# Performance work log

Hardware: AMD Instinct MI355X
Metric: run time of the kernel (lower is better)

The kernel has to match this reference:

```python
import jax, jax.numpy as jnp
import numpy as np

LEN = 8388608  # 2**23, must be a power of 2


def setup_inputs() -> dict:
    key = jax.random.key(0)
    k1, k2 = jax.random.split(key)
    inp = jax.random.normal(k1, (LEN,), dtype=jnp.float32)
    weight = jax.random.uniform(k2, (LEN // 2, 2), dtype=jnp.float32)  # learned twiddle factors
    return {"input": inp, "weight": weight}


def _complex_mul(a, w):
    # a: [d, cols, 2] complex pairs; w: [cols, 2] broadcast over leading dim
    ar, ai = a[:, :, 0], a[:, :, 1]
    wr, wi = w[:, 0], w[:, 1]
    return jnp.stack([ar * wr - ai * wi, ar * wi + ai * wr], axis=-1)


def reference(input, weight):
    n = input.shape[0]
    # real signal -> complex pairs, shape [n, 1, 2]
    x = jnp.stack([input, jnp.zeros_like(input)], axis=-1)[:, None, :]
    d = n // 2
    while d != 0:  # log2(n) static stages
        w = weight[0::d]          # [cols, 2] where cols == x.shape[1]
        top = x[:d]               # [d, cols, 2]
        bot = x[d:]               # [d, cols, 2]
        p = _complex_mul(bot, w)  # butterfly twiddle multiply
        x = jnp.concatenate([top + p, top - p], axis=1)  # [d, 2*cols, 2]
        d //= 2
    return x  # [1, n, 2]
```

## Files before the change

### kernel.cpp

```cpp
#include <hip/hip_runtime.h>
#include <hip/hip_fp16.h>

__device__ __forceinline__ float2 cadd(float2 a, float2 b) { return make_float2(a.x + b.x, a.y + b.y); }
__device__ __forceinline__ float2 csub(float2 a, float2 b) { return make_float2(a.x - b.x, a.y - b.y); }
__device__ __forceinline__ float2 cmul(float2 w, float2 z) {
    return make_float2(w.x * z.x - w.y * z.y, w.x * z.y + w.y * z.x);
}
__device__ __forceinline__ unsigned pk(float2 z) {
    __half2 h = __floats2half2_rn(z.x, z.y);
    return *reinterpret_cast<unsigned*>(&h);
}
__device__ __forceinline__ float2 upk(unsigned u) {
    __half2 h = *reinterpret_cast<__half2*>(&u);
    return __half22float2(h);
}


__global__ __launch_bounds__(256) void fft_pass_a(const float* __restrict__ in,
                                                  const float2* __restrict__ wt,
                                                  uint4* __restrict__ outp)
{
    __shared__ float2 L[4096];
    const int tid = threadIdx.x;
    const int l0  = blockIdx.x << 4;
    const int c   = tid & 15;
    const int qb  = tid >> 4;

    float2 pw1[4], pw2a[4], pw2b[4];
#pragma unroll
    for (int k = 0; k < 4; ++k) { pw1[k] = wt[0]; pw2a[k] = wt[0]; pw2b[k] = wt[1 << 21]; }

    {
        const int c4 = tid & 3, gg = tid >> 2;
#pragma unroll
        for (int k = 0; k < 4; ++k) {
            const int g = gg + (k << 6);
            const float4 v = *reinterpret_cast<const float4*>(in + ((size_t)g << 15) + l0 + (c4 << 2));
            const int base = (g << 4) + (c4 << 2);
            L[base + 0] = make_float2(v.x, 0.f);
            L[base + 1] = make_float2(v.y, 0.f);
            L[base + 2] = make_float2(v.z, 0.f);
            L[base + 3] = make_float2(v.w, 0.f);
        }
    }
    __syncthreads();

#pragma unroll
    for (int rho = 0; rho < 4; ++rho) {
        const int s = rho << 1, H = 128 >> s, Q = H >> 1, lo = 6 - s;
        float2 nw1[4], nw2a[4], nw2b[4];
        if (rho < 3) {
            const int s2 = s + 2, lo2 = 6 - s2;
#pragma unroll
            for (int k = 0; k < 4; ++k) {
                const int qi = (qb << 2) + k;
                const int b  = ((qi >> lo2) << (lo2 + 2)) | (qi & ((1 << lo2) - 1));
                const int jl = (int)(__brev((unsigned)(b >> (8 - s2))) >> (32 - s2));
                const int e  = jl << (21 - s2);
                nw1[k] = wt[e << 1]; nw2a[k] = wt[e]; nw2b[k] = wt[e + (1 << 21)];
            }
        }
#pragma unroll
        for (int k = 0; k < 4; ++k) {
            const int qi = (qb << 2) + k;
            const int b  = ((qi >> lo) << (lo + 2)) | (qi & ((1 << lo) - 1));
            const int iA = (b << 4) + c;
            const float2 A  = L[iA];
            const float2 Bv = L[iA + (Q << 4)];
            const float2 Cv = L[iA + (H << 4)];
            const float2 Dv = L[iA + ((H + Q) << 4)];
            const float2 pC = cmul(pw1[k], Cv), pD = cmul(pw1[k], Dv);
            const float2 tA = cadd(A, pC),  tC = csub(A, pC);
            const float2 tB = cadd(Bv, pD), tD = csub(Bv, pD);
            const float2 p2 = cmul(pw2a[k], tB);
            const float2 p3 = cmul(pw2b[k], tD);
            L[iA]                  = cadd(tA, p2);
            L[iA + (Q << 4)]       = csub(tA, p2);
            L[iA + (H << 4)]       = cadd(tC, p3);
            L[iA + ((H + Q) << 4)] = csub(tC, p3);
        }
        __syncthreads();
        if (rho < 3) {
#pragma unroll
            for (int k = 0; k < 4; ++k) { pw1[k] = nw1[k]; pw2a[k] = nw2a[k]; pw2b[k] = nw2b[k]; }
        }
    }

    {
        const int c4 = tid & 3, gg = tid >> 2;
#pragma unroll
        for (int k = 0; k < 4; ++k) {
            const int g  = gg + (k << 6);
            const int li = (g << 4) + (c4 << 2);
            uint4 v;
            v.x = pk(L[li]); v.y = pk(L[li + 1]); v.z = pk(L[li + 2]); v.w = pk(L[li + 3]);
            outp[((size_t)g << 13) + (l0 >> 2) + c4] = v;
        }
    }
}

__global__ __launch_bounds__(256) void fft_pass_b(const uint4* __restrict__ inp,
                                                  const float2* __restrict__ wt,
                                                  uint4* __restrict__ outp)
{
    __shared__ float2 L[4096];
    const int tid  = threadIdx.x;
    const int h    = blockIdx.x >> 3;
    const int l0   = (blockIdx.x & 7) << 4;
    const int hrev = (int)(__brev((unsigned)h) >> 24);
    const int c  = tid & 15;
    const int qb = tid >> 4;
    const size_t pbase = ((size_t)h << 13) + (l0 >> 2);

    float2 pw1[4], pw2a[4], pw2b[4];
    {
        const int e0 = hrev << 13;
#pragma unroll
        for (int k = 0; k < 4; ++k) { pw1[k] = wt[e0 << 1]; pw2a[k] = wt[e0]; pw2b[k] = wt[e0 + (1 << 21)]; }
    }

    {
        const int c4 = tid & 3, gg = tid >> 2;
#pragma unroll
        for (int k = 0; k < 4; ++k) {
            const int g = gg + (k << 6);
            const uint4 v = inp[pbase + (g << 5) + c4];
            const int li = (g << 4) + (c4 << 2);
            L[li]     = upk(v.x);
            L[li + 1] = upk(v.y);
            L[li + 2] = upk(v.z);
            L[li + 3] = upk(v.w);
        }
    }
    __syncthreads();

#pragma unroll
    for (int rho = 0; rho < 4; ++rho) {
        const int s = rho << 1, H = 128 >> s, Q = H >> 1, lo = 6 - s;
        float2 nw1[4], nw2a[4], nw2b[4];
        if (rho < 3) {
            const int s2 = s + 2, lo2 = 6 - s2;
#pragma unroll
            for (int k = 0; k < 4; ++k) {
                const int qi = (qb << 2) + k;
                const int b  = ((qi >> lo2) << (lo2 + 2)) | (qi & ((1 << lo2) - 1));
                const int jl = (int)(__brev((unsigned)(b >> (8 - s2))) >> (32 - s2));
                const int e  = (hrev << (13 - s2)) + (jl << (21 - s2));
                nw1[k] = wt[e << 1]; nw2a[k] = wt[e]; nw2b[k] = wt[e + (1 << 21)];
            }
        }
#pragma unroll
        for (int k = 0; k < 4; ++k) {
            const int qi = (qb << 2) + k;
            const int b  = ((qi >> lo) << (lo + 2)) | (qi & ((1 << lo) - 1));
            const int iA = (b << 4) + c;
            const float2 A  = L[iA];
            const float2 Bv = L[iA + (Q << 4)];
            const float2 Cv = L[iA + (H << 4)];
            const float2 Dv = L[iA + ((H + Q) << 4)];
            const float2 pC = cmul(pw1[k], Cv), pD = cmul(pw1[k], Dv);
            const float2 tA = cadd(A, pC),  tC = csub(A, pC);
            const float2 tB = cadd(Bv, pD), tD = csub(Bv, pD);
            const float2 p2 = cmul(pw2a[k], tB);
            const float2 p3 = cmul(pw2b[k], tD);
            L[iA]                  = cadd(tA, p2);
            L[iA + (Q << 4)]       = csub(tA, p2);
            L[iA + (H << 4)]       = cadd(tC, p3);
            L[iA + ((H + Q) << 4)] = csub(tC, p3);
        }
        __syncthreads();
        if (rho < 3) {
#pragma unroll
            for (int k = 0; k < 4; ++k) { pw1[k] = nw1[k]; pw2a[k] = nw2a[k]; pw2b[k] = nw2b[k]; }
        }
    }

    {
        const int c4 = tid & 3, gg = tid >> 2;
#pragma unroll
        for (int k = 0; k < 4; ++k) {
            const int g  = gg + (k << 6);
            const int li = (g << 4) + (c4 << 2);
            uint4 v;
            v.x = pk(L[li]); v.y = pk(L[li + 1]); v.z = pk(L[li + 2]); v.w = pk(L[li + 3]);
            outp[pbase + (g << 5) + c4] = v;
        }
    }
}

__global__ __launch_bounds__(256, 8) void fft_pass_c(const uint4* __restrict__ inp,
                                                     const float2* __restrict__ wt,
                                                     float2* __restrict__ out)
{
    __shared__ float2 L[16 * 129];
    const int tid = threadIdx.x;
    const int h0  = blockIdx.x;

    const int lam = tid & 15;
    const int bq  = tid >> 4;
    const int rH  = (h0 << 4) + lam;

    float2 pw1[2], pw2a[2], pw2b[2];
#pragma unroll
    for (int k = 0; k < 2; ++k) {
        pw1[k]  = wt[rH << 6];
        pw2a[k] = wt[rH << 5];
        pw2b[k] = wt[(rH << 5) + (1 << 21)];
    }

    {
        const int f  = tid & 31;
        const int ll = tid >> 5;
#pragma unroll
        for (int k = 0; k < 2; ++k) {
            const int lm = ll + (k << 3);
            const int H  = (int)(__brev((unsigned)((h0 << 4) + lm)) >> 16);
            const uint4 v = inp[((size_t)H << 5) + f];
            const int li = lm * 129 + (f << 2);
            L[li]     = upk(v.x);
            L[li + 1] = upk(v.y);
            L[li + 2] = upk(v.z);
            L[li + 3] = upk(v.w);
        }
    }
    __syncthreads();

    float2 pr2[4];
#pragma unroll
    for (int rho = 0; rho < 3; ++rho) {
        const int s = rho << 1, H = 64 >> s, Q = H >> 1, lo = 5 - s;
        float2 nw1[2], nw2a[2], nw2b[2];
        if (rho < 2) {
            const int s2 = s + 2, lo2 = 5 - s2;
#pragma unroll
            for (int k = 0; k < 2; ++k) {
                const int qi = (bq << 1) + k;
                const int b  = ((qi >> lo2) << (lo2 + 2)) | (qi & ((1 << lo2) - 1));
                const int jl = (int)(__brev((unsigned)(b >> (7 - s2))) >> (32 - s2));
                const int e  = (rH << (5 - s2)) + (jl << (21 - s2));
                nw1[k] = wt[e << 1]; nw2a[k] = wt[e]; nw2b[k] = wt[e + (1 << 21)];
            }
        } else {
#pragma unroll
            for (int k = 0; k < 4; ++k) {
                const int pb = (bq << 2) + k;
                const int jl = (int)(__brev((unsigned)pb) >> 26);
                pr2[k] = wt[rH + (jl << 16)];
            }
        }
#pragma unroll
        for (int k = 0; k < 2; ++k) {
            const int qi = (bq << 1) + k;
            const int b  = ((qi >> lo) << (lo + 2)) | (qi & ((1 << lo) - 1));
            const int iA = lam * 129 + b;
            const float2 A  = L[iA];
            const float2 Bv = L[iA + Q];
            const float2 Cv = L[iA + H];
            const float2 Dv = L[iA + H + Q];
            const float2 pC = cmul(pw1[k], Cv), pD = cmul(pw1[k], Dv);
            const float2 tA = cadd(A, pC),  tC = csub(A, pC);
            const float2 tB = cadd(Bv, pD), tD = csub(Bv, pD);
            const float2 p2 = cmul(pw2a[k], tB);
            const float2 p3 = cmul(pw2b[k], tD);
            L[iA]         = cadd(tA, p2);
            L[iA + Q]     = csub(tA, p2);
            L[iA + H]     = cadd(tC, p3);
            L[iA + H + Q] = csub(tC, p3);
        }
        __syncthreads();
        if (rho < 2) {
#pragma unroll
            for (int k = 0; k < 2; ++k) { pw1[k] = nw1[k]; pw2a[k] = nw2a[k]; pw2b[k] = nw2b[k]; }
        }
    }

    {
#pragma unroll
        for (int k = 0; k < 4; ++k) {
            const int pb = (bq << 2) + k;
            const int b  = pb << 1;
            const int iA = lam * 129 + b;
            const float2 A  = L[iA];
            const float2 Bv = L[iA + 1];
            const float2 p  = cmul(pr2[k], Bv);
            L[iA]     = cadd(A, p);
            L[iA + 1] = csub(A, p);
        }
    }
    __syncthreads();

    {
        const int l2 = (tid & 7) << 1;
        const int gb = tid >> 3;
#pragma unroll
        for (int k = 0; k < 4; ++k) {
            const int g    = gb + (k << 5);
            const int grev = (int)(__brev((unsigned)g) >> 25);
            const float2 a0 = L[l2 * 129 + g];
            const float2 a1 = L[(l2 + 1) * 129 + g];
            const size_t o = ((size_t)grev << 16) + (h0 << 4) + l2;
            *reinterpret_cast<float4*>(out + o) = make_float4(a0.x, a0.y, a1.x, a1.y);
        }
    }
}

extern "C" void kernel_launch(void* const* d_in, const int* in_sizes, int n_in,
                              void* d_out, int out_size, void* d_ws, size_t ws_size,
                              hipStream_t stream)
{
    (void)in_sizes; (void)n_in; (void)out_size; (void)ws_size;
    const float*  in = (const float*)d_in[0];
    const float2* wt = (const float2*)d_in[1];
    float2* outc = (float2*)d_out;
    uint4*  buf1 = (uint4*)d_ws;
    uint4*  buf2 = (uint4*)((char*)d_ws + (32u << 20));

    fft_pass_a<<<2048, 256, 0, stream>>>(in,   wt, buf1);
    fft_pass_b<<<2048, 256, 0, stream>>>(buf1, wt, buf2);
    fft_pass_c<<<4096, 256, 0, stream>>>(buf2, wt, outc);
}
```

Baseline: 180.6 us.

## Widen pass A tile to 32 columns with fp16 packed padded shared memory

Pass A now processes 32 columns per block instead of 16, so it launches half as many blocks. Its shared-memory tile holds fp16-packed complex values with a stride-33 pad to avoid bank conflicts. Twiddle prefetching across stages is dropped; twiddles are loaded inline from global memory for each butterfly. Rounding to fp16 between the in-block stages lowers precision, and each thread now does 8 butterflies per stage, which raises per-thread work and latency exposure.

```diff
diff --git a/kernel.cpp b/kernel.cpp
--- a/kernel.cpp
+++ b/kernel.cpp
@@ -10,6 +10,10 @@
     __half2 h = __floats2half2_rn(z.x, z.y);
     return *reinterpret_cast<unsigned*>(&h);
 }
+__device__ __forceinline__ unsigned pkr(float x) {
+    __half2 h = __floats2half2_rn(x, 0.f);
+    return *reinterpret_cast<unsigned*>(&h);
+}
 __device__ __forceinline__ float2 upk(unsigned u) {
     __half2 h = *reinterpret_cast<__half2*>(&u);
     return __half22float2(h);
@@ -20,81 +24,66 @@
                                                   const float2* __restrict__ wt,
                                                   uint4* __restrict__ outp)
 {
-    __shared__ float2 L[4096];
+    __shared__ unsigned Lp[256 * 33];
     const int tid = threadIdx.x;
-    const int l0  = blockIdx.x << 4;
-    const int c   = tid & 15;
-    const int qb  = tid >> 4;
-
-    float2 pw1[4], pw2a[4], pw2b[4];
-#pragma unroll
-    for (int k = 0; k < 4; ++k) { pw1[k] = wt[0]; pw2a[k] = wt[0]; pw2b[k] = wt[1 << 21]; }
-
-    {
-        const int c4 = tid & 3, gg = tid >> 2;
-#pragma unroll
-        for (int k = 0; k < 4; ++k) {
-            const int g = gg + (k << 6);
-            const float4 v = *reinterpret_cast<const float4*>(in + ((size_t)g << 15) + l0 + (c4 << 2));
-            const int base = (g << 4) + (c4 << 2);
-            L[base + 0] = make_float2(v.x, 0.f);
-            L[base + 1] = make_float2(v.y, 0.f);
-            L[base + 2] = make_float2(v.z, 0.f);
-            L[base + 3] = make_float2(v.w, 0.f);
+    const int l0  = blockIdx.x << 5;
+
+    {
+        const int f4 = tid & 7, g8 = tid >> 3;
+#pragma unroll
+        for (int k = 0; k < 8; ++k) {
+            const int g = g8 + (k << 5);
+            const float4 v = *reinterpret_cast<const float4*>(in + ((size_t)g << 15) + l0 + (f4 << 2));
+            const int base = g * 33 + (f4 << 2);
+            Lp[base + 0] = pkr(v.x);
+            Lp[base + 1] = pkr(v.y);
+            Lp[base + 2] = pkr(v.z);
+            Lp[base + 3] = pkr(v.w);
         }
     }
     __syncthreads();
 
+    const int c  = tid & 31;
+    const int qb = tid >> 5;
 #pragma unroll
     for (int rho = 0; rho < 4; ++rho) {
         const int s = rho << 1, H = 128 >> s, Q = H >> 1, lo = 6 - s;
-        float2 nw1[4], nw2a[4], nw2b[4];
-        if (rho < 3) {
-            const int s2 = s + 2, lo2 = 6 - s2;
-#pragma unroll
-            for (int k = 0; k < 4; ++k) {
-                const int qi = (qb << 2) + k;
-                const int b  = ((qi >> lo2) << (lo2 + 2)) | (qi & ((1 << lo2) - 1));
-                const int jl = (int)(__brev((unsigned)(b >> (8 - s2))) >> (32 - s2));
-                const int e  = jl << (21 - s2);
-                nw1[k] = wt[e << 1]; nw2a[k] = wt[e]; nw2b[k] = wt[e + (1 << 21)];
-            }
-        }
-#pragma unroll
-        for (int k = 0; k < 4; ++k) {
-            const int qi = (qb << 2) + k;
+#pragma unroll
+        for (int k = 0; k < 8; ++k) {
+            const int qi = (qb << 3) + k;
             const int b  = ((qi >> lo) << (lo + 2)) | (qi & ((1 << lo) - 1));
-            const int iA = (b << 4) + c;
-            const float2 A  = L[iA];
-            const float2 Bv = L[iA + (Q << 4)];
-            const float2 Cv = L[iA + (H << 4)];
-            const float2 Dv = L[iA + ((H + Q) << 4)];
-            const float2 pC = cmul(pw1[k], Cv), pD = cmul(pw1[k], Dv);
+            const int jl = s ? (int)(__brev((unsigned)(b >> (8 - s))) >> (32 - s)) : 0;
+            const int e  = jl << (21 - s);
+            const float2 w1  = wt[e << 1];
+            const float2 w2a = wt[e];
+            const float2 w2b = wt[e + (1 << 21)];
+            const int iA = b * 33 + c;
+            const float2 A  = upk(Lp[iA]);
+            const float2 Bv = upk(Lp[iA + Q * 33]);
+            const float2 Cv = upk(Lp[iA + H * 33]);
+            const float2 Dv = upk(Lp[iA + (H + Q) * 33]);
+            const float2 pC = cmul(w1, Cv), pD = cmul(w1, Dv);
             const float2 tA = cadd(A, pC),  tC = csub(A, pC);
             const float2 tB = cadd(Bv, pD), tD = csub(Bv, pD);
-            const float2 p2 = cmul(pw2a[k], tB);
-            const float2 p3 = cmul(pw2b[k], tD);
-            L[iA]                  = cadd(tA, p2);
-            L[iA + (Q << 4)]       = csub(tA, p2);
-            L[iA + (H << 4)]       = cadd(tC, p3);
-            L[iA + ((H + Q) << 4)] = csub(tC, p3);
+            const float2 p2 = cmul(w2a, tB);
+            const float2 p3 = cmul(w2b, tD);
+            Lp[iA]                = pk(cadd(tA, p2));
+            Lp[iA + Q * 33]       = pk(csub(tA, p2));
+            Lp[iA + H * 33]       = pk(cadd(tC, p3));
+            Lp[iA + (H + Q) * 33] = pk(csub(tC, p3));
         }
         __syncthreads();
-        if (rho < 3) {
-#pragma unroll
-            for (int k = 0; k < 4; ++k) { pw1[k] = nw1[k]; pw2a[k] = nw2a[k]; pw2b[k] = nw2b[k]; }
-        }
-    }
-
-    {
-        const int c4 = tid & 3, gg = tid >> 2;
-#pragma unroll
-        for (int k = 0; k < 4; ++k) {
-            const int g  = gg + (k << 6);
-            const int li = (g << 4) + (c4 << 2);
+    }
+
+    {
+        const int f4 = tid & 7, g8 = tid >> 3;
+#pragma unroll
+        for (int k = 0; k < 8; ++k) {
+            const int g    = g8 + (k << 5);
+            const int base = g * 33 + (f4 << 2);
             uint4 v;
-            v.x = pk(L[li]); v.y = pk(L[li + 1]); v.z = pk(L[li + 2]); v.w = pk(L[li + 3]);
-            outp[((size_t)g << 13) + (l0 >> 2) + c4] = v;
+            v.x = Lp[base]; v.y = Lp[base + 1]; v.z = Lp[base + 2]; v.w = Lp[base + 3];
+            outp[((size_t)g << 13) + (l0 >> 2) + f4] = v;
         }
     }
 }
@@ -315,7 +304,7 @@
     uint4*  buf1 = (uint4*)d_ws;
     uint4*  buf2 = (uint4*)((char*)d_ws + (32u << 20));
 
-    fft_pass_a<<<2048, 256, 0, stream>>>(in,   wt, buf1);
+    fft_pass_a<<<1024, 256, 0, stream>>>(in,   wt, buf1);
     fft_pass_b<<<2048, 256, 0, stream>>>(buf1, wt, buf2);
     fft_pass_c<<<4096, 256, 0, stream>>>(buf2, wt, outc);
 }
```

Result: no change. 180.7 us (+0.1%).
